# Performance work log

Hardware: AMD Instinct MI355X
Metric: run time of the kernel (lower is better)

## Reference

```python
import jax, jax.numpy as jnp
import numpy as np

TIME_STEPS = 8

def setup_inputs() -> dict:
    key = jax.random.key(0)
    feature_matrix = jax.random.normal(key, (64, 1, 1000, 128), dtype=jnp.float32)
    return {"feature_matrix": feature_matrix}

def reference(feature_matrix):
    # squeeze channel -> (B, F, Bd)
    x = jnp.squeeze(feature_matrix, axis=1)
    min_val = jnp.min(x, axis=(1, 2), keepdims=True)
    max_val = jnp.max(x, axis=(1, 2), keepdims=True)
    norm = TIME_STEPS * (x - min_val) / (max_val - min_val)  # values in [0, 8]
    # The torch loop (mask = v > 0; store; v[mask] -= 1) is exactly equivalent to
    # mask_t = (norm > t) for t = 0..TIME_STEPS-1, since once v <= 0 it never
    # becomes positive again. Vectorize over the time axis in one pass.
    t = jnp.arange(TIME_STEPS, dtype=norm.dtype)  # (T,)
    spikes = (norm[..., None] > t).astype(jnp.float32)  # (B, F, Bd, T)
    # torch.randperm shuffle of time axis; use a fixed permutation for determinism
    perm = jax.random.permutation(jax.random.key(1), TIME_STEPS)
    spikes = spikes[..., perm]
    return spikes[:, None]  # (B, 1, F, Bd, T)
```

## Files before the change

kernel.cpp:

```cpp
#include <hip/hip_runtime.h>
#include <cstdint>
#include <cstddef>


typedef float f32x4 __attribute__((ext_vector_type(4)));

struct TF2 { uint32_t a, b; };

constexpr uint32_t rotl32(uint32_t x, int d) { return (x << d) | (x >> (32 - d)); }

constexpr TF2 threefry2x32(uint32_t k0, uint32_t k1, uint32_t x0, uint32_t x1) {
  const uint32_t ks2 = k0 ^ k1 ^ 0x1BD11BDAu;
  const int R0[4] = {13, 15, 26, 6};
  const int R1[4] = {17, 29, 16, 24};
  x0 += k0; x1 += k1;
  for (int i = 0; i < 4; ++i) { x0 += x1; x1 = rotl32(x1, R0[i]); x1 ^= x0; }
  x0 += k1; x1 += ks2 + 1u;
  for (int i = 0; i < 4; ++i) { x0 += x1; x1 = rotl32(x1, R1[i]); x1 ^= x0; }
  x0 += ks2; x1 += k0 + 2u;
  for (int i = 0; i < 4; ++i) { x0 += x1; x1 = rotl32(x1, R0[i]); x1 ^= x0; }
  x0 += k0; x1 += k1 + 3u;
  for (int i = 0; i < 4; ++i) { x0 += x1; x1 = rotl32(x1, R1[i]); x1 ^= x0; }
  x0 += k1; x1 += ks2 + 4u;
  for (int i = 0; i < 4; ++i) { x0 += x1; x1 = rotl32(x1, R0[i]); x1 ^= x0; }
  x0 += ks2; x1 += k0 + 5u;
  return TF2{x0, x1};
}

struct Perm { int p[8]; };

constexpr Perm compute_perm() {
  TF2 s = threefry2x32(0u, 1u, 0u, 1u);
  uint32_t sk0 = s.a, sk1 = s.b;
  uint32_t bits[8] = {};
  for (int i = 0; i < 8; ++i) {
    TF2 r = threefry2x32(sk0, sk1, 0u, (uint32_t)i);
    bits[i] = r.a ^ r.b;
  }
  Perm perm = {{0, 1, 2, 3, 4, 5, 6, 7}};
  for (int i = 1; i < 8; ++i) {
    uint32_t kb = bits[i]; int kv = perm.p[i];
    int j = i - 1;
    while (j >= 0 && bits[j] > kb) { bits[j + 1] = bits[j]; perm.p[j + 1] = perm.p[j]; --j; }
    bits[j + 1] = kb; perm.p[j + 1] = kv;
  }
  return perm;
}

constexpr Perm PERM = compute_perm();

static constexpr int B = 64;
static constexpr int PER_BATCH = 1000 * 128;
static constexpr int PER_BATCH_F4 = PER_BATCH / 4;
static constexpr int MM_BLOCKS_PER_BATCH = 16;
static constexpr int MM_F4_PER_BLOCK = PER_BATCH_F4 / MM_BLOCKS_PER_BATCH;

static constexpr int ENC_OUT4_PER_BLOCK = 2048;
static constexpr int ENC_BLOCKS = 16384000 / ENC_OUT4_PER_BLOCK;
static constexpr int ENC_BLOCKS_PER_BATCH = 125;

__device__ inline uint32_t f2key(float f) {
  uint32_t u = __float_as_uint(f);
  return (u & 0x80000000u) ? ~u : (u | 0x80000000u);
}
__device__ inline float key2f(uint32_t k) {
  uint32_t u = (k & 0x80000000u) ? (k & 0x7FFFFFFFu) : ~k;
  return __uint_as_float(u);
}

__global__ __launch_bounds__(128) void init_keys(uint32_t* keys) {
  int i = threadIdx.x;
  keys[i] = (i & 1) ? 0u : 0xFFFFFFFFu;
}

__global__ __launch_bounds__(256) void minmax_kernel(const float4* __restrict__ in,
                                                     uint32_t* __restrict__ keys) {
  const int batch = blockIdx.x >> 4;
  const int sub = blockIdx.x & 15;
  const float4* bp = in + (size_t)batch * PER_BATCH_F4;
  float mn = INFINITY, mx = -INFINITY;
  const int end = (sub + 1) * MM_F4_PER_BLOCK;
  for (int i = sub * MM_F4_PER_BLOCK + threadIdx.x; i < end; i += 256) {
    float4 v = bp[i];
    mn = fminf(mn, fminf(fminf(v.x, v.y), fminf(v.z, v.w)));
    mx = fmaxf(mx, fmaxf(fmaxf(v.x, v.y), fmaxf(v.z, v.w)));
  }
  #pragma unroll
  for (int off = 32; off > 0; off >>= 1) {
    mn = fminf(mn, __shfl_down(mn, off));
    mx = fmaxf(mx, __shfl_down(mx, off));
  }
  __shared__ float smn[4], smx[4];
  const int wave = threadIdx.x >> 6, lane = threadIdx.x & 63;
  if (lane == 0) { smn[wave] = mn; smx[wave] = mx; }
  __syncthreads();
  if (threadIdx.x == 0) {
    mn = fminf(fminf(smn[0], smn[1]), fminf(smn[2], smn[3]));
    mx = fmaxf(fmaxf(smx[0], smx[1]), fmaxf(smx[2], smx[3]));
    atomicMin(&keys[2 * batch], f2key(mn));
    atomicMax(&keys[2 * batch + 1], f2key(mx));
  }
}

__global__ __launch_bounds__(256) void encode_kernel(const float* __restrict__ in,
                                                     f32x4* __restrict__ out,
                                                     const uint32_t* __restrict__ keys) {
  const int batch = blockIdx.x / ENC_BLOCKS_PER_BATCH;
  const float mn = key2f(keys[2 * batch]);
  const float mx = key2f(keys[2 * batch + 1]);
  const float rng = mx - mn;

  const int p = (threadIdx.x & 1) * 4;
  const float th0 = (float)PERM.p[p + 0];
  const float th1 = (float)PERM.p[p + 1];
  const float th2 = (float)PERM.p[p + 2];
  const float th3 = (float)PERM.p[p + 3];

  const int out4_base = blockIdx.x * ENC_OUT4_PER_BLOCK + threadIdx.x;
  #pragma unroll
  for (int k = 0; k < 8; ++k) {
    const int o4 = out4_base + k * 256;
    const float x = in[o4 >> 1];
    const float n = (8.0f * (x - mn)) / rng;
    f32x4 o;
    o.x = n > th0 ? 1.0f : 0.0f;
    o.y = n > th1 ? 1.0f : 0.0f;
    o.z = n > th2 ? 1.0f : 0.0f;
    o.w = n > th3 ? 1.0f : 0.0f;
    __builtin_nontemporal_store(o, &out[o4]);
  }
}

extern "C" void kernel_launch(void* const* d_in, const int* in_sizes, int n_in,
                              void* d_out, int out_size, void* d_ws, size_t ws_size,
                              hipStream_t stream) {
  const float* in = (const float*)d_in[0];
  f32x4* out = (f32x4*)d_out;
  uint32_t* keys = (uint32_t*)d_ws;

  hipLaunchKernelGGL(init_keys, dim3(1), dim3(128), 0, stream, keys);
  hipLaunchKernelGGL(minmax_kernel, dim3(B * MM_BLOCKS_PER_BATCH), dim3(256), 0, stream,
                     (const float4*)in, keys);
  hipLaunchKernelGGL(encode_kernel, dim3(ENC_BLOCKS), dim3(256), 0, stream,
                     in, out, keys);
}
```

Before: 285.3 us.

## Fuse min/max reduction and spike encoding into one cooperative kernel

Replaces the three launches (key init, atomic min/max, encode) with one cooperative kernel. Each of the 1024 blocks writes a partial min/max, the whole grid synchronises, then each block reduces its batch's 16 partials and encodes its own slice of the output. This removes two kernel launches and the atomics, and each block's minmax slice lines up with the input its encode slice reads, so that data may still be in cache. In exchange it adds a grid-wide barrier, requires all 1024 blocks to be resident at once, and uses far fewer blocks for the large write phase.

```diff
diff --git a/kernel.cpp b/kernel.cpp
--- a/kernel.cpp
+++ b/kernel.cpp
@@ -1,7 +1,10 @@
 #include <hip/hip_runtime.h>
+#include <hip/hip_cooperative_groups.h>
 #include <cstdint>
 #include <cstddef>
 
+
+namespace cg = cooperative_groups;
 
 typedef float f32x4 __attribute__((ext_vector_type(4)));
 
@@ -50,34 +53,20 @@
 constexpr Perm PERM = compute_perm();
 
 static constexpr int B = 64;
-static constexpr int PER_BATCH = 1000 * 128;
-static constexpr int PER_BATCH_F4 = PER_BATCH / 4;
-static constexpr int MM_BLOCKS_PER_BATCH = 16;
-static constexpr int MM_F4_PER_BLOCK = PER_BATCH_F4 / MM_BLOCKS_PER_BATCH;
+static constexpr int PER_BATCH_F4 = 32000;
+static constexpr int BLOCKS_PER_BATCH = 16;
+static constexpr int GRID_BLOCKS = B * BLOCKS_PER_BATCH;
+static constexpr int MM_F4_PER_BLOCK = PER_BATCH_F4 / BLOCKS_PER_BATCH;
+static constexpr int OUT4_PER_BLOCK = 16000;
 
-static constexpr int ENC_OUT4_PER_BLOCK = 2048;
-static constexpr int ENC_BLOCKS = 16384000 / ENC_OUT4_PER_BLOCK;
-static constexpr int ENC_BLOCKS_PER_BATCH = 125;
+__global__ __launch_bounds__(256, 4) void fused_encoder(const float* __restrict__ in,
+                                                        f32x4* __restrict__ out,
+                                                        float* __restrict__ part) {
+  const int blk = blockIdx.x;
+  const int batch = blk >> 4;
+  const int sub = blk & 15;
 
-__device__ inline uint32_t f2key(float f) {
-  uint32_t u = __float_as_uint(f);
-  return (u & 0x80000000u) ? ~u : (u | 0x80000000u);
-}
-__device__ inline float key2f(uint32_t k) {
-  uint32_t u = (k & 0x80000000u) ? (k & 0x7FFFFFFFu) : ~k;
-  return __uint_as_float(u);
-}
-
-__global__ __launch_bounds__(128) void init_keys(uint32_t* keys) {
-  int i = threadIdx.x;
-  keys[i] = (i & 1) ? 0u : 0xFFFFFFFFu;
-}
-
-__global__ __launch_bounds__(256) void minmax_kernel(const float4* __restrict__ in,
-                                                     uint32_t* __restrict__ keys) {
-  const int batch = blockIdx.x >> 4;
-  const int sub = blockIdx.x & 15;
-  const float4* bp = in + (size_t)batch * PER_BATCH_F4;
+  const float4* bp = (const float4*)in + (size_t)batch * PER_BATCH_F4;
   float mn = INFINITY, mx = -INFINITY;
   const int end = (sub + 1) * MM_F4_PER_BLOCK;
   for (int i = sub * MM_F4_PER_BLOCK + threadIdx.x; i < end; i += 256) {
@@ -97,18 +86,28 @@
   if (threadIdx.x == 0) {
     mn = fminf(fminf(smn[0], smn[1]), fminf(smn[2], smn[3]));
     mx = fmaxf(fmaxf(smx[0], smx[1]), fmaxf(smx[2], smx[3]));
-    atomicMin(&keys[2 * batch], f2key(mn));
-    atomicMax(&keys[2 * batch + 1], f2key(mx));
+    __hip_atomic_store(&part[2 * blk],     mn, __ATOMIC_RELAXED, __HIP_MEMORY_SCOPE_AGENT);
+    __hip_atomic_store(&part[2 * blk + 1], mx, __ATOMIC_RELAXED, __HIP_MEMORY_SCOPE_AGENT);
   }
-}
 
-__global__ __launch_bounds__(256) void encode_kernel(const float* __restrict__ in,
-                                                     f32x4* __restrict__ out,
-                                                     const uint32_t* __restrict__ keys) {
-  const int batch = blockIdx.x / ENC_BLOCKS_PER_BATCH;
-  const float mn = key2f(keys[2 * batch]);
-  const float mx = key2f(keys[2 * batch + 1]);
-  const float rng = mx - mn;
+  cg::this_grid().sync();
+
+  __shared__ float s_red[2];
+  if (threadIdx.x < 16) {
+    float pmn = __hip_atomic_load(&part[2 * (batch * 16 + threadIdx.x)],
+                                  __ATOMIC_RELAXED, __HIP_MEMORY_SCOPE_AGENT);
+    float pmx = __hip_atomic_load(&part[2 * (batch * 16 + threadIdx.x) + 1],
+                                  __ATOMIC_RELAXED, __HIP_MEMORY_SCOPE_AGENT);
+    #pragma unroll
+    for (int off = 8; off > 0; off >>= 1) {
+      pmn = fminf(pmn, __shfl_down(pmn, off));
+      pmx = fmaxf(pmx, __shfl_down(pmx, off));
+    }
+    if (threadIdx.x == 0) { s_red[0] = pmn; s_red[1] = pmx; }
+  }
+  __syncthreads();
+  const float bmn = s_red[0];
+  const float rng = s_red[1] - bmn;
 
   const int p = (threadIdx.x & 1) * 4;
   const float th0 = (float)PERM.p[p + 0];
@@ -116,12 +115,12 @@
   const float th2 = (float)PERM.p[p + 2];
   const float th3 = (float)PERM.p[p + 3];
 
-  const int out4_base = blockIdx.x * ENC_OUT4_PER_BLOCK + threadIdx.x;
-  #pragma unroll
-  for (int k = 0; k < 8; ++k) {
-    const int o4 = out4_base + k * 256;
+  const int out4_base = blk * OUT4_PER_BLOCK;
+  #pragma unroll 4
+  for (int i = threadIdx.x; i < OUT4_PER_BLOCK; i += 256) {
+    const int o4 = out4_base + i;
     const float x = in[o4 >> 1];
-    const float n = (8.0f * (x - mn)) / rng;
+    const float n = (8.0f * (x - bmn)) / rng;
     f32x4 o;
     o.x = n > th0 ? 1.0f : 0.0f;
     o.y = n > th1 ? 1.0f : 0.0f;
@@ -136,11 +135,9 @@
                               hipStream_t stream) {
   const float* in = (const float*)d_in[0];
   f32x4* out = (f32x4*)d_out;
-  uint32_t* keys = (uint32_t*)d_ws;
+  float* part = (float*)d_ws;
 
-  hipLaunchKernelGGL(init_keys, dim3(1), dim3(128), 0, stream, keys);
-  hipLaunchKernelGGL(minmax_kernel, dim3(B * MM_BLOCKS_PER_BATCH), dim3(256), 0, stream,
-                     (const float4*)in, keys);
-  hipLaunchKernelGGL(encode_kernel, dim3(ENC_BLOCKS), dim3(256), 0, stream,
-                     in, out, keys);
+  void* args[3] = {(void*)&in, (void*)&out, (void*)&part};
+  hipLaunchCooperativeKernel((const void*)fused_encoder, dim3(GRID_BLOCKS), dim3(256),
+                             args, 0, stream);
 }
```

Result: slower. 415.1 us (+45.5%).
